# Optimization experiments

Measured on AMD Instinct MI355X. Metric: run time of the kernel, lower is better.

Reference implementation:

```python
import jax, jax.numpy as jnp
import numpy as np

DIM = 1024
NUM_HEADS = 16
HEAD_DIM = DIM // NUM_HEADS
SCALE = HEAD_DIM ** -0.5


def setup_inputs() -> dict:
    key = jax.random.key(0)
    k1, k2, k3 = jax.random.split(key, 3)
    x = jax.random.normal(k1, (2, 2048, DIM), dtype=jnp.float32)
    # nn.Linear weights: stored as [out, in]; y = x @ W.T
    w_qkv = jax.random.normal(k2, (3 * DIM, DIM), dtype=jnp.float32) * (DIM ** -0.5)
    w_proj = jax.random.normal(k3, (DIM, DIM), dtype=jnp.float32) * (DIM ** -0.5)
    return {"x": x, "w_qkv": w_qkv, "w_proj": w_proj}


def reference(x, w_qkv, w_proj):
    B, L, D = x.shape
    qkv = jnp.einsum("bld,ed->ble", x, w_qkv)  # [B, L, 3*D]
    qkv = qkv.reshape(B, L, 3, NUM_HEADS, HEAD_DIM).transpose(2, 0, 3, 1, 4)
    q, k, v = qkv[0], qkv[1], qkv[2]  # each [B, H, L, hd]
    attn = jnp.einsum("bhqd,bhkd->bhqk", q, k) * SCALE
    attn = jax.nn.softmax(attn, axis=-1)
    out = jnp.einsum("bhqk,bhkd->bhqd", attn, v)  # [B, H, L, hd]
    out = out.transpose(0, 2, 1, 3).reshape(B, L, D)
    return jnp.einsum("bld,ed->ble", out, w_proj)
```

## Files before the change

### kernel.cpp

```cpp
#include <hip/hip_runtime.h>
#include <math.h>
#include <stdint.h>

#define B_ 2
#define L_ 2048
#define D_ 1024
#define H_ 16
#define HD_ 64
#define QSCALE_ 0.1803368801f

typedef __attribute__((ext_vector_type(8))) short short8;
typedef __attribute__((ext_vector_type(4))) short short4v;
typedef __attribute__((ext_vector_type(4))) float float4v;

#if defined(__has_builtin)
#if __has_builtin(__builtin_amdgcn_exp2f)
#define EXP2F(x) __builtin_amdgcn_exp2f(x)
#endif
#endif
#ifndef EXP2F
#define EXP2F(x) exp2f(x)
#endif

__device__ __forceinline__ short f2bf(float f) {
    union { float f; unsigned u; } x; x.f = f;
    unsigned r = x.u + 0x7fffu + ((x.u >> 16) & 1u);
    return (short)(r >> 16);
}

__device__ __forceinline__ void gl_lds16(const void* g, void* l) {
    __builtin_amdgcn_global_load_lds(
        (const __attribute__((address_space(1))) unsigned int*)g,
        (__attribute__((address_space(3))) unsigned int*)l, 16, 0, 0);
}

__global__ __launch_bounds__(256) void cvt_bf16(const float* __restrict__ in,
                                                short* __restrict__ out, int n4) {
    int i = blockIdx.x * 256 + threadIdx.x;
    if (i >= n4) return;
    float4 v = ((const float4*)in)[i];
    short4v o;
    o.x = f2bf(v.x); o.y = f2bf(v.y); o.z = f2bf(v.z); o.w = f2bf(v.w);
    ((short4v*)out)[i] = o;
}

__global__ __launch_bounds__(256) void gemm_qkv_bf16(const short* __restrict__ A,
                                                     const short* __restrict__ Bm,
                                                     short* __restrict__ Qb,
                                                     short* __restrict__ Kb,
                                                     short* __restrict__ Vb) {
    __shared__ short smem[8192];
    short* As = smem;
    short* Bs = smem + 4096;
    const int tid = threadIdx.x;
    const int w = tid >> 6, l = tid & 63;
    const int lm = l & 15, q = l >> 4;
    const int m0 = blockIdx.y * 128, n0 = blockIdx.x * 128;
    const int wm = w >> 1, wn = w & 1;

    float4v acc[4][4];
#pragma unroll
    for (int mt = 0; mt < 4; ++mt)
#pragma unroll
        for (int nt = 0; nt < 4; ++nt) acc[mt][nt] = (float4v){0.f, 0.f, 0.f, 0.f};

    for (int k0 = 0; k0 < 1024; k0 += 32) {
        __syncthreads();
#pragma unroll
        for (int t = 0; t < 2; ++t) {
            int idx8 = w * 128 + t * 64 + l;
            int row = idx8 >> 2, c8 = idx8 & 3;
            gl_lds16(A  + (size_t)(m0 + row) * 1024 + k0 + c8 * 8, (char*)As + w * 2048 + t * 1024);
            gl_lds16(Bm + (size_t)(n0 + row) * 1024 + k0 + c8 * 8, (char*)Bs + w * 2048 + t * 1024);
        }
        __syncthreads();
        short8 af[4], bfr[4];
#pragma unroll
        for (int mt = 0; mt < 4; ++mt)
            af[mt] = *(const short8*)(As + (wm * 64 + mt * 16 + lm) * 32 + q * 8);
#pragma unroll
        for (int nt = 0; nt < 4; ++nt)
            bfr[nt] = *(const short8*)(Bs + (wn * 64 + nt * 16 + lm) * 32 + q * 8);
#pragma unroll
        for (int mt = 0; mt < 4; ++mt)
#pragma unroll
            for (int nt = 0; nt < 4; ++nt)
                acc[mt][nt] = __builtin_amdgcn_mfma_f32_16x16x32_bf16(af[mt], bfr[nt], acc[mt][nt], 0, 0, 0);
    }

    const int which = n0 >> 10;
    if (which < 2) {
        short* dst = (which == 0) ? Qb : Kb;
        const float sc = (which == 0) ? QSCALE_ : 1.0f;
#pragma unroll
        for (int half = 0; half < 2; ++half) {
            __syncthreads();
            if (wm == half) {
#pragma unroll
                for (int mt = 0; mt < 4; ++mt)
#pragma unroll
                    for (int nt = 0; nt < 4; ++nt)
#pragma unroll
                        for (int r = 0; r < 4; ++r)
                            smem[(mt * 16 + q * 4 + r) * 128 + wn * 64 + nt * 16 + lm] =
                                f2bf(acc[mt][nt][r] * sc);
            }
            __syncthreads();
#pragma unroll
            for (int j = 0; j < 4; ++j) {
                const int x = tid + 256 * j;
                const int row = x >> 4, c = x & 15;
                short8 v = *(const short8*)(smem + row * 128 + c * 8);
                const int m = m0 + half * 64 + row;
                const int b = m >> 11, ll = m & 2047;
                const int n = n0 + c * 8;
                const int hh = (n & 1023) >> 6, d = n & 63;
                *(short8*)(dst + (((size_t)b * H_ + hh) * L_ + ll) * HD_ + d) = v;
            }
        }
    } else {
#pragma unroll
        for (int mt = 0; mt < 4; ++mt) {
            const int m = m0 + wm * 64 + mt * 16 + q * 4;
            const int b = m >> 11, ll = m & 2047;
#pragma unroll
            for (int nt = 0; nt < 4; ++nt) {
                const int n = n0 + wn * 64 + nt * 16 + lm;
                const int h = (n & 1023) >> 6, d = n & 63;
                short4v pk;
                pk.x = f2bf(acc[mt][nt][0]); pk.y = f2bf(acc[mt][nt][1]);
                pk.z = f2bf(acc[mt][nt][2]); pk.w = f2bf(acc[mt][nt][3]);
                *(short4v*)(Vb + (((size_t)b * H_ + h) * HD_ + d) * L_ + ll) = pk;
            }
        }
    }
}

__global__ __launch_bounds__(256) void attn_mfma(const short* __restrict__ Qb,
                                                 const short* __restrict__ Kb,
                                                 const short* __restrict__ Vtg,
                                                 short* __restrict__ Ob) {
    __shared__ short Ql[128 * 64];
    __shared__ short KV[4 * 4096];
    __shared__ short Pt[128 * 72];

    const int tid = threadIdx.x;
    const int w = tid >> 6, l = tid & 63;
    const int lm = l & 15, q = l >> 4;
    const int qt = blockIdx.x, bh = blockIdx.y;

    const short* Qg = Qb  + ((size_t)bh * L_ + qt * 128) * HD_;
    const short* Kg = Kb  + (size_t)bh * L_ * HD_;
    const short* Vg = Vtg + (size_t)bh * HD_ * L_;

#pragma unroll
    for (int t = 0; t < 4; ++t) {
        int idx = tid + 256 * t;
        int row = idx >> 3, c = idx & 7;
        short8 v = *(const short8*)(Qg + row * 64 + c * 8);
        *(short8*)(Ql + row * 64 + ((c ^ (row & 7)) * 8)) = v;
    }

    const int srow = tid >> 3;
    const int sc   = tid & 7;
    const int koff0 = srow * 64 + ((sc ^ (srow & 7)) * 8);
    const int koff1 = koff0 + 32 * 64;

    {
        short8 ka = *(const short8*)(Kg + (size_t)srow * 64 + sc * 8);
        short8 kb = *(const short8*)(Kg + (size_t)(srow + 32) * 64 + sc * 8);
        short8 va = *(const short8*)(Vg + (size_t)srow * L_ + sc * 8);
        short8 vb = *(const short8*)(Vg + (size_t)(srow + 32) * L_ + sc * 8);
        *(short8*)(KV + koff0) = ka;
        *(short8*)(KV + koff1) = kb;
        *(short8*)(KV + 4096 + koff0) = va;
        *(short8*)(KV + 4096 + koff1) = vb;
    }
    short8 kra = *(const short8*)(Kg + (size_t)(64 + srow) * 64 + sc * 8);
    short8 krb = *(const short8*)(Kg + (size_t)(64 + srow + 32) * 64 + sc * 8);
    short8 vra = *(const short8*)(Vg + (size_t)srow * L_ + 64 + sc * 8);
    short8 vrb = *(const short8*)(Vg + (size_t)(srow + 32) * L_ + 64 + sc * 8);

    __syncthreads();

    short8 qf[2][2];
#pragma unroll
    for (int nq = 0; nq < 2; ++nq)
#pragma unroll
        for (int kh = 0; kh < 2; ++kh) {
            int row = w * 32 + nq * 16 + lm;
            int ch = kh * 4 + q;
            qf[nq][kh] = *(const short8*)(Ql + row * 64 + ((ch ^ (row & 7)) * 8));
        }

    int offA0[4], offA1[4], offV[2][4];
#pragma unroll
    for (int nt = 0; nt < 4; ++nt) {
        const int arow = nt * 16 + lm;
        offA0[nt] = arow * 64 + ((q ^ (arow & 7)) * 8);
        offA1[nt] = arow * 64 + (((4 + q) ^ (arow & 7)) * 8);
#pragma unroll
        for (int kh = 0; kh < 2; ++kh)
            offV[kh][nt] = arow * 64 + (((kh * 4 + q) ^ (arow & 7)) * 8);
    }

    float4v o[4][2];
#pragma unroll
    for (int mt = 0; mt < 4; ++mt)
#pragma unroll
        for (int nq = 0; nq < 2; ++nq) o[mt][nq] = (float4v){0.f, 0.f, 0.f, 0.f};
    float lsum[2] = {0.f, 0.f};

    const int prow = w * 32 + lm;

#pragma unroll 2
    for (int t = 0; t < 32; ++t) {
        const int cur = t & 1;
        short* Kl = KV + cur * 8192;
        short* Vt = Kl + 4096;
        short* Kn = KV + (1 - cur) * 8192;
        short* Vn = Kn + 4096;

        __syncthreads();

        if (t < 31) {
            *(short8*)(Kn + koff0) = kra;
            *(short8*)(Kn + koff1) = krb;
            *(short8*)(Vn + koff0) = vra;
            *(short8*)(Vn + koff1) = vrb;
        }
        if (t < 30) {
            kra = *(const short8*)(Kg + (size_t)((t + 2) * 64 + srow) * 64 + sc * 8);
            krb = *(const short8*)(Kg + (size_t)((t + 2) * 64 + srow + 32) * 64 + sc * 8);
            vra = *(const short8*)(Vg + (size_t)srow * L_ + (t + 2) * 64 + sc * 8);
            vrb = *(const short8*)(Vg + (size_t)(srow + 32) * L_ + (t + 2) * 64 + sc * 8);
        }

        float4v st[4][2];
#pragma unroll
        for (int nt = 0; nt < 4; ++nt) {
            short8 a0 = *(const short8*)(Kl + offA0[nt]);
            short8 a1 = *(const short8*)(Kl + offA1[nt]);
#pragma unroll
            for (int nq = 0; nq < 2; ++nq) {
                float4v z = (float4v){0.f, 0.f, 0.f, 0.f};
                z = __builtin_amdgcn_mfma_f32_16x16x32_bf16(a0, qf[nq][0], z, 0, 0, 0);
                z = __builtin_amdgcn_mfma_f32_16x16x32_bf16(a1, qf[nq][1], z, 0, 0, 0);
                st[nt][nq] = z;
            }
        }

#pragma unroll
        for (int nt = 0; nt < 4; ++nt)
#pragma unroll
            for (int nq = 0; nq < 2; ++nq) {
                const float e0 = EXP2F(st[nt][nq][0]);
                const float e1 = EXP2F(st[nt][nq][1]);
                const float e2 = EXP2F(st[nt][nq][2]);
                const float e3 = EXP2F(st[nt][nq][3]);
                lsum[nq] += (e0 + e1) + (e2 + e3);
                short4v pk;
                pk.x = f2bf(e0); pk.y = f2bf(e1); pk.z = f2bf(e2); pk.w = f2bf(e3);
                *(short4v*)(Pt + (prow + nq * 16) * 72 + nt * 16 + q * 4) = pk;
            }

#pragma unroll
        for (int kh = 0; kh < 2; ++kh) {
            short8 pb[2];
#pragma unroll
            for (int nq = 0; nq < 2; ++nq)
                pb[nq] = *(const short8*)(Pt + (prow + nq * 16) * 72 + kh * 32 + q * 8);
#pragma unroll
            for (int mt = 0; mt < 4; ++mt) {
                short8 va = *(const short8*)(Vt + offV[kh][mt]);
#pragma unroll
                for (int nq = 0; nq < 2; ++nq)
                    o[mt][nq] = __builtin_amdgcn_mfma_f32_16x16x32_bf16(va, pb[nq], o[mt][nq], 0, 0, 0);
            }
        }
    }

    float inv[2];
#pragma unroll
    for (int nq = 0; nq < 2; ++nq) {
        float s = lsum[nq];
        s += __shfl_xor(s, 16);
        s += __shfl_xor(s, 32);
        inv[nq] = 1.f / s;
    }
    short* OgBase = Ob + ((size_t)bh * L_ + qt * 128) * HD_;
#pragma unroll
    for (int nq = 0; nq < 2; ++nq) {
        const int qrow = w * 32 + nq * 16 + lm;
#pragma unroll
        for (int mt = 0; mt < 4; ++mt) {
            short4v pk;
            pk.x = f2bf(o[mt][nq][0] * inv[nq]);
            pk.y = f2bf(o[mt][nq][1] * inv[nq]);
            pk.z = f2bf(o[mt][nq][2] * inv[nq]);
            pk.w = f2bf(o[mt][nq][3] * inv[nq]);
            *(short4v*)(OgBase + (size_t)qrow * 64 + mt * 16 + q * 4) = pk;
        }
    }
}

__global__ __launch_bounds__(256) void gemm_proj_bf16(const short* __restrict__ Ob,
                                                      const short* __restrict__ Wp,
                                                      float* __restrict__ out) {
    __shared__ short As[64 * 32];
    __shared__ short Bs[128 * 32];
    const int tid = threadIdx.x;
    const int w = tid >> 6, l = tid & 63;
    const int lm = l & 15, q = l >> 4;
    const int m0 = blockIdx.y * 64, n0 = blockIdx.x * 128;
    const int wm = w & 1, wn = w >> 1;
    const int b = m0 >> 11, l0 = m0 & 2047;

    float4v acc[2][4];
#pragma unroll
    for (int mt = 0; mt < 2; ++mt)
#pragma unroll
        for (int nt = 0; nt < 4; ++nt) acc[mt][nt] = (float4v){0.f, 0.f, 0.f, 0.f};

    for (int k0 = 0; k0 < 1024; k0 += 32) {
        __syncthreads();
        {
            int idx8 = w * 64 + l;
            int row = idx8 >> 2, c8 = idx8 & 3;
            int h = k0 >> 6, d = (k0 & 32) + c8 * 8;
            gl_lds16(Ob + (((size_t)b * H_ + h) * L_ + l0 + row) * HD_ + d, (char*)As + w * 1024);
        }
#pragma unroll
        for (int t = 0; t < 2; ++t) {
            int idx8 = w * 128 + t * 64 + l;
            int row = idx8 >> 2, c8 = idx8 & 3;
            gl_lds16(Wp + (size_t)(n0 + row) * 1024 + k0 + c8 * 8, (char*)Bs + w * 2048 + t * 1024);
        }
        __syncthreads();
        short8 af[2], bfr[4];
#pragma unroll
        for (int mt = 0; mt < 2; ++mt)
            af[mt] = *(const short8*)(As + (wm * 32 + mt * 16 + lm) * 32 + q * 8);
#pragma unroll
        for (int nt = 0; nt < 4; ++nt)
            bfr[nt] = *(const short8*)(Bs + (wn * 64 + nt * 16 + lm) * 32 + q * 8);
#pragma unroll
        for (int mt = 0; mt < 2; ++mt)
#pragma unroll
            for (int nt = 0; nt < 4; ++nt)
                acc[mt][nt] = __builtin_amdgcn_mfma_f32_16x16x32_bf16(af[mt], bfr[nt], acc[mt][nt], 0, 0, 0);
    }

#pragma unroll
    for (int mt = 0; mt < 2; ++mt)
#pragma unroll
        for (int nt = 0; nt < 4; ++nt)
#pragma unroll
            for (int r = 0; r < 4; ++r) {
                const int m = m0 + wm * 32 + mt * 16 + q * 4 + r;
                const int n = n0 + wn * 64 + nt * 16 + lm;
                out[(size_t)m * 1024 + n] = acc[mt][nt][r];
            }
}

extern "C" void kernel_launch(void* const* d_in, const int* in_sizes, int n_in,
                              void* d_out, int out_size, void* d_ws, size_t ws_size,
                              hipStream_t stream) {
    (void)in_sizes; (void)n_in; (void)out_size; (void)ws_size;
    const float* x      = (const float*)d_in[0];
    const float* w_qkv  = (const float*)d_in[1];
    const float* w_proj = (const float*)d_in[2];

    char* ws = (char*)d_ws;
    short* xb     = (short*)(ws);
    short* wqkvb  = (short*)(ws + (8u  << 20));
    short* wprojb = (short*)(ws + (14u << 20));
    short* Qb     = (short*)(ws + (16u << 20));
    short* Kb     = (short*)(ws + (24u << 20));
    short* Vb     = (short*)(ws + (32u << 20));
    short* Ob     = xb;

    cvt_bf16<<<4096, 256, 0, stream>>>(x,      xb,     1048576);
    cvt_bf16<<<3072, 256, 0, stream>>>(w_qkv,  wqkvb,   786432);
    cvt_bf16<<<1024, 256, 0, stream>>>(w_proj, wprojb,  262144);
    gemm_qkv_bf16 <<<dim3(24, 32), 256, 0, stream>>>(xb, wqkvb, Qb, Kb, Vb);
    attn_mfma     <<<dim3(16, 32), 256, 0, stream>>>(Qb, Kb, Vb, Ob);
    gemm_proj_bf16<<<dim3(8, 64),  256, 0, stream>>>(Ob, wprojb, (float*)d_out);
}
```

Measured before the change: 201.0 us.

## Fuse x bf16 conversion into QKV GEMM, merge weight casts, alias Q LDS

```diff
diff --git a/kernel.cpp b/kernel.cpp
--- a/kernel.cpp
+++ b/kernel.cpp
@@ -28,23 +28,38 @@
     return (short)(r >> 16);
 }
 
+__device__ __forceinline__ unsigned fbits(float f) {
+    union { float f; unsigned u; } x; x.f = f;
+    return x.u;
+}
+
+__device__ __forceinline__ unsigned pk_bf_trunc(float a, float b) {
+    return __builtin_amdgcn_perm(fbits(b), fbits(a), 0x07060302u);
+}
+
 __device__ __forceinline__ void gl_lds16(const void* g, void* l) {
     __builtin_amdgcn_global_load_lds(
         (const __attribute__((address_space(1))) unsigned int*)g,
         (__attribute__((address_space(3))) unsigned int*)l, 16, 0, 0);
 }
 
-__global__ __launch_bounds__(256) void cvt_bf16(const float* __restrict__ in,
-                                                short* __restrict__ out, int n4) {
+__global__ __launch_bounds__(256) void cvt_w(const float* __restrict__ wqkv,
+                                             const float* __restrict__ wproj,
+                                             short* __restrict__ wqkvb,
+                                             short* __restrict__ wprojb) {
     int i = blockIdx.x * 256 + threadIdx.x;
-    if (i >= n4) return;
-    float4 v = ((const float4*)in)[i];
+    const float* in;
+    short* out;
+    int idx;
+    if (i < 786432) { in = wqkv;  out = wqkvb;  idx = i; }
+    else            { in = wproj; out = wprojb; idx = i - 786432; }
+    float4 v = ((const float4*)in)[idx];
     short4v o;
     o.x = f2bf(v.x); o.y = f2bf(v.y); o.z = f2bf(v.z); o.w = f2bf(v.w);
-    ((short4v*)out)[i] = o;
-}
-
-__global__ __launch_bounds__(256) void gemm_qkv_bf16(const short* __restrict__ A,
+    ((short4v*)out)[idx] = o;
+}
+
+__global__ __launch_bounds__(256) void gemm_qkv_bf16(const float* __restrict__ X,
                                                      const short* __restrict__ Bm,
                                                      short* __restrict__ Qb,
                                                      short* __restrict__ Kb,
@@ -58,22 +73,46 @@
     const int m0 = blockIdx.y * 128, n0 = blockIdx.x * 128;
     const int wm = w >> 1, wn = w & 1;
 
+    int arow_[4], acol_[4];
+#pragma unroll
+    for (int j = 0; j < 4; ++j) {
+        int c = tid + 256 * j;
+        arow_[j] = c >> 3;
+        acol_[j] = (c & 7) * 4;
+    }
+
     float4v acc[4][4];
 #pragma unroll
     for (int mt = 0; mt < 4; ++mt)
 #pragma unroll
         for (int nt = 0; nt < 4; ++nt) acc[mt][nt] = (float4v){0.f, 0.f, 0.f, 0.f};
+
+    float4 areg[4];
+#pragma unroll
+    for (int j = 0; j < 4; ++j)
+        areg[j] = *(const float4*)(X + (size_t)(m0 + arow_[j]) * 1024 + acol_[j]);
 
     for (int k0 = 0; k0 < 1024; k0 += 32) {
         __syncthreads();
+#pragma unroll
+        for (int j = 0; j < 4; ++j) {
+            short4v s4;
+            s4.x = f2bf(areg[j].x); s4.y = f2bf(areg[j].y);
+            s4.z = f2bf(areg[j].z); s4.w = f2bf(areg[j].w);
+            *(short4v*)(As + arow_[j] * 32 + acol_[j]) = s4;
+        }
 #pragma unroll
         for (int t = 0; t < 2; ++t) {
             int idx8 = w * 128 + t * 64 + l;
             int row = idx8 >> 2, c8 = idx8 & 3;
-            gl_lds16(A  + (size_t)(m0 + row) * 1024 + k0 + c8 * 8, (char*)As + w * 2048 + t * 1024);
             gl_lds16(Bm + (size_t)(n0 + row) * 1024 + k0 + c8 * 8, (char*)Bs + w * 2048 + t * 1024);
         }
         __syncthreads();
+        if (k0 < 992) {
+#pragma unroll
+            for (int j = 0; j < 4; ++j)
+                areg[j] = *(const float4*)(X + (size_t)(m0 + arow_[j]) * 1024 + k0 + 32 + acol_[j]);
+        }
         short8 af[4], bfr[4];
 #pragma unroll
         for (int mt = 0; mt < 4; ++mt)
@@ -140,7 +179,6 @@
                                                  const short* __restrict__ Kb,
                                                  const short* __restrict__ Vtg,
                                                  short* __restrict__ Ob) {
-    __shared__ short Ql[128 * 64];
     __shared__ short KV[4 * 4096];
     __shared__ short Pt[128 * 72];
 
@@ -158,7 +196,7 @@
         int idx = tid + 256 * t;
         int row = idx >> 3, c = idx & 7;
         short8 v = *(const short8*)(Qg + row * 64 + c * 8);
-        *(short8*)(Ql + row * 64 + ((c ^ (row & 7)) * 8)) = v;
+        *(short8*)(Pt + row * 64 + ((c ^ (row & 7)) * 8)) = v;
     }
 
     const int srow = tid >> 3;
@@ -190,7 +228,7 @@
         for (int kh = 0; kh < 2; ++kh) {
             int row = w * 32 + nq * 16 + lm;
             int ch = kh * 4 + q;
-            qf[nq][kh] = *(const short8*)(Ql + row * 64 + ((ch ^ (row & 7)) * 8));
+            qf[nq][kh] = *(const short8*)(Pt + row * 64 + ((ch ^ (row & 7)) * 8));
         }
 
     int offA0[4], offA1[4], offV[2][4];
@@ -259,9 +297,10 @@
                 const float e2 = EXP2F(st[nt][nq][2]);
                 const float e3 = EXP2F(st[nt][nq][3]);
                 lsum[nq] += (e0 + e1) + (e2 + e3);
-                short4v pk;
-                pk.x = f2bf(e0); pk.y = f2bf(e1); pk.z = f2bf(e2); pk.w = f2bf(e3);
-                *(short4v*)(Pt + (prow + nq * 16) * 72 + nt * 16 + q * 4) = pk;
+                uint2 pk;
+                pk.x = pk_bf_trunc(e0, e1);
+                pk.y = pk_bf_trunc(e2, e3);
+                *(uint2*)(Pt + (prow + nq * 16) * 72 + nt * 16 + q * 4) = pk;
             }
 
 #pragma unroll
@@ -372,18 +411,15 @@
     const float* w_proj = (const float*)d_in[2];
 
     char* ws = (char*)d_ws;
-    short* xb     = (short*)(ws);
+    short* Ob     = (short*)(ws);
     short* wqkvb  = (short*)(ws + (8u  << 20));
     short* wprojb = (short*)(ws + (14u << 20));
     short* Qb     = (short*)(ws + (16u << 20));
     short* Kb     = (short*)(ws + (24u << 20));
     short* Vb     = (short*)(ws + (32u << 20));
-    short* Ob     = xb;
-
-    cvt_bf16<<<4096, 256, 0, stream>>>(x,      xb,     1048576);
-    cvt_bf16<<<3072, 256, 0, stream>>>(w_qkv,  wqkvb,   786432);
-    cvt_bf16<<<1024, 256, 0, stream>>>(w_proj, wprojb,  262144);
-    gemm_qkv_bf16 <<<dim3(24, 32), 256, 0, stream>>>(xb, wqkvb, Qb, Kb, Vb);
+
+    cvt_w<<<4096, 256, 0, stream>>>(w_qkv, w_proj, wqkvb, wprojb);
+    gemm_qkv_bf16 <<<dim3(24, 32), 256, 0, stream>>>(x, wqkvb, Qb, Kb, Vb);
     attn_mfma     <<<dim3(16, 32), 256, 0, stream>>>(Qb, Kb, Vb, Ob);
     gemm_proj_bf16<<<dim3(8, 64),  256, 0, stream>>>(Ob, wprojb, (float*)d_out);
 }
```

New measurement: 208.5 us. 1.04x slower.
